# Kernel tuning notes

Measured on AMD Instinct MI355X. Metric: run time of the kernel, lower is better.

## Reference

```python
import jax, jax.numpy as jnp
import numpy as np

STATE_DIM, GOAL_DIM, OBST_DIM = 6, 3, 4
VEH_DIM = 2 * STATE_DIM + GOAL_DIM          # 15
IN_DIM = VEH_DIM + OBST_DIM                 # 19
HIDDEN = 256
ACT_DIM = 2
ACT_LIMIT = 1.0
LOG_STD_MIN, LOG_STD_MAX = -20.0, 2.0


def setup_inputs() -> dict:
    key = jax.random.key(0)
    ks = jax.random.split(key, 12)
    B, N = 512, 256
    sc = lambda fan_in: 1.0 / np.sqrt(fan_in)
    return {
        "obs": jax.random.normal(ks[0], (B, VEH_DIM), jnp.float32),
        "obstacles": jax.random.uniform(ks[1], (B, OBST_DIM + 1, N), jnp.float32),
        "eps": jax.random.normal(ks[2], (B, ACT_DIM), jnp.float32),
        "W1": jax.random.normal(ks[3], (IN_DIM, HIDDEN), jnp.float32) * sc(IN_DIM),
        "b1": jnp.zeros((HIDDEN,), jnp.float32),
        "W2": jax.random.normal(ks[4], (HIDDEN, HIDDEN), jnp.float32) * sc(HIDDEN),
        "b2": jnp.zeros((HIDDEN,), jnp.float32),
        "mu_W": jax.random.normal(ks[5], (HIDDEN, ACT_DIM), jnp.float32) * sc(HIDDEN),
        "mu_b": jnp.zeros((ACT_DIM,), jnp.float32),
        "ls_W": jax.random.normal(ks[6], (HIDDEN, ACT_DIM), jnp.float32) * sc(HIDDEN),
        "ls_b": jnp.zeros((ACT_DIM,), jnp.float32),
    }


def reference(obs, obstacles, eps, W1, b1, W2, b2, mu_W, mu_b, ls_W, ls_b):
    B, _, N = obstacles.shape
    # gather/expand/concat: [B, N, 19]
    veh = jnp.broadcast_to(obs[:, None, :], (B, N, VEH_DIM))
    obst_feats = jnp.swapaxes(obstacles[:, :OBST_DIM, :], 1, 2)  # [B, N, 4]
    x = jnp.concatenate([veh, obst_feats], axis=-1)
    # shared per-obstacle MLP (message function)
    h = jax.nn.relu(x @ W1 + b1)
    h = jax.nn.relu(h @ W2 + b2)                                 # [B, N, H]
    # masked sum pooling (aggregation)
    mask = obstacles[:, -1, :]                                   # [B, N]
    pooled = jnp.einsum('bnh,bn->bh', h, mask)                   # [B, H]
    # Gaussian tanh-squash head
    mu = pooled @ mu_W + mu_b
    log_std = jnp.clip(pooled @ ls_W + ls_b, LOG_STD_MIN, LOG_STD_MAX)
    std = jnp.exp(log_std)
    a = mu + std * eps  # rsample with externally supplied noise
    # Normal log_prob(a) with a = mu + std*eps  ->  -0.5*eps^2 - log_std - 0.5*log(2pi)
    logp = jnp.sum(-0.5 * eps * eps - log_std - 0.5 * jnp.log(2.0 * jnp.pi), axis=-1)
    # tanh correction
    logp = logp - jnp.sum(2.0 * (jnp.log(2.0) - a - jax.nn.softplus(-2.0 * a)), axis=-1)
    pi_action = ACT_LIMIT * jnp.tanh(a)
    return pi_action, logp
```

## Files before the change

### kernel.cpp

```cpp
#include <hip/hip_runtime.h>
#include <math.h>

typedef __attribute__((ext_vector_type(8))) short short8;
typedef __attribute__((ext_vector_type(4))) float f32x4;

__device__ __forceinline__ unsigned short f2bf(float x) {
    unsigned u = __float_as_uint(x);
    u += 0x7FFFu + ((u >> 16) & 1u);
    return (unsigned short)(u >> 16);
}

#define A1P_OFF 131072

__global__ __launch_bounds__(256) void prep_kernel(const float* __restrict__ W2,
                                                   const float* __restrict__ W1,
                                                   unsigned short* __restrict__ W2p,
                                                   unsigned short* __restrict__ A1p) {
    const int t = threadIdx.x;
    const int blk = blockIdx.x;
    if (blk < 32) {
        int f = blk * 256 + t;
        int l = f & 63, ct = (f >> 6) & 15, kt = f >> 10;
        int col = ct * 16 + (l & 15);
        int krow = kt * 32 + ((l >> 4) * 8);
        short8 v;
#pragma unroll
        for (int j = 0; j < 8; ++j) v[j] = (short)f2bf(W2[(krow + j) * 256 + col]);
        *reinterpret_cast<short8*>(W2p + (size_t)f * 8) = v;
    } else {
        int f = (blk - 32) * 256 + t;
        int l = f & 63, jt = f >> 6;
        int j = jt * 16 + (l & 15);
        short8 v;
#pragma unroll
        for (int jj = 0; jj < 8; ++jj) {
            int k = (l >> 4) * 8 + jj;
            v[jj] = (k < 4) ? (short)f2bf(W1[(15 + k) * 256 + j]) : (short)0;
        }
        *reinterpret_cast<short8*>(A1p + (size_t)f * 8) = v;
    }
}

__global__ __launch_bounds__(512, 2) void actor_kernel(
    const float* __restrict__ obs,  const float* __restrict__ obst,
    const float* __restrict__ W1,   const float* __restrict__ b1,
    const float* __restrict__ b2,   const unsigned short* __restrict__ W2p,
    const unsigned short* __restrict__ A1p,
    const float* __restrict__ muW,  const float* __restrict__ lsW,
    const float* __restrict__ mub,  const float* __restrict__ lsb,
    const float* __restrict__ eps,  float* __restrict__ out)
{
    __shared__ __align__(16) short sA[4 * 64 * 64];
    __shared__ float sVeh[256];
    __shared__ float sRed[8][4];

    const int b = blockIdx.x;
    const int t = threadIdx.x;
    const int l = t & 63;
    const int w = t >> 6;
    const int g = l >> 4;
    const int ln = l & 15;

    if (t < 256) {
        float a = b1[t];
#pragma unroll
        for (int i = 0; i < 15; ++i) a = fmaf(obs[b * 15 + i], W1[i * 256 + t], a);
        sVeh[t] = a;
    }

    short8 bfr[8][2];
#pragma unroll
    for (int kt = 0; kt < 8; ++kt)
#pragma unroll
        for (int c = 0; c < 2; ++c)
            bfr[kt][c] = *reinterpret_cast<const short8*>(
                W2p + (size_t)(((kt * 16 + (w * 2 + c)) * 64 + l) * 8));

    short8 a1[2];
#pragma unroll
    for (int ji = 0; ji < 2; ++ji)
        a1[ji] = *reinterpret_cast<const short8*>(
            A1p + (size_t)(((w * 2 + ji) * 64 + l) * 8));

    float bb[2]; float2 mwv[2], lwv[2];
#pragma unroll
    for (int c = 0; c < 2; ++c) {
        int col = w * 32 + c * 16 + ln;
        bb[c] = b2[col];
        mwv[c] = *reinterpret_cast<const float2*>(muW + col * 2);
        lwv[c] = *reinterpret_cast<const float2*>(lsW + col * 2);
    }

    const float* ob = obst + b * 1280;
    const float* maskbase = ob + 1024;

    short8 bf1[4];
    auto loadB1 = [&](int q) {
#pragma unroll
        for (int nt = 0; nt < 4; ++nt) {
            short8 v = {0, 0, 0, 0, 0, 0, 0, 0};
            if (l < 16) {
#pragma unroll
                for (int jj = 0; jj < 4; ++jj)
                    v[jj] = (short)f2bf(ob[jj * 256 + q * 64 + nt * 16 + l]);
            }
            bf1[nt] = v;
        }
    };
    loadB1(0);

    f32x4 acc[4][2];
#pragma unroll
    for (int m = 0; m < 4; ++m)
#pragma unroll
        for (int c = 0; c < 2; ++c) acc[m][c] = (f32x4){0.f, 0.f, 0.f, 0.f};
    float m0 = 0.f, m1 = 0.f, s0 = 0.f, s1 = 0.f;

    __syncthreads();

    for (int q = 0; q < 4; ++q) {
#pragma unroll
        for (int ji = 0; ji < 2; ++ji) {
            int jt = w * 2 + ji;
            int j0 = jt * 16 + g * 4;
            f32x4 bias = *reinterpret_cast<const f32x4*>(&sVeh[j0]);
            unsigned page = (unsigned)(j0 >> 6) * 8192;
            unsigned jbyte = (unsigned)((j0 & 63) * 2);
#pragma unroll
            for (int nt = 0; nt < 4; ++nt) {
                f32x4 d = (f32x4){0.f, 0.f, 0.f, 0.f};
                d = __builtin_amdgcn_mfma_f32_16x16x32_bf16(a1[ji], bf1[nt], d, 0, 0, 0);
                int n = nt * 16 + ln;
                unsigned p0 = (unsigned)f2bf(fmaxf(d[0] + bias[0], 0.f));
                unsigned p1 = (unsigned)f2bf(fmaxf(d[1] + bias[1], 0.f));
                unsigned p2 = (unsigned)f2bf(fmaxf(d[2] + bias[2], 0.f));
                unsigned p3 = (unsigned)f2bf(fmaxf(d[3] + bias[3], 0.f));
                uint2 u;
                u.x = p0 | (p1 << 16);
                u.y = p2 | (p3 << 16);
                unsigned off = page + (unsigned)(n * 128) + (jbyte ^ ((unsigned)((n & 7) << 4)));
                *reinterpret_cast<uint2*>((char*)sA + off) = u;
            }
        }
        if (q < 3) loadB1(q + 1);
        __syncthreads();

#pragma unroll
        for (int kt = 0; kt < 8; ++kt) {
            unsigned page = (unsigned)(kt >> 1) * 8192;
            unsigned kbyte = (unsigned)((kt & 1) * 64 + g * 16);
#pragma unroll
            for (int m = 0; m < 4; ++m) {
                int n = m * 16 + ln;
                unsigned off = page + (unsigned)(n * 128) + (kbyte ^ ((unsigned)((n & 7) << 4)));
                short8 afr = *reinterpret_cast<const short8*>((const char*)sA + off);
#pragma unroll
                for (int c = 0; c < 2; ++c)
                    acc[m][c] = __builtin_amdgcn_mfma_f32_16x16x32_bf16(afr, bfr[kt][c], acc[m][c], 0, 0, 0);
            }
        }

        const float* maskp = maskbase + q * 64;
#pragma unroll
        for (int c = 0; c < 2; ++c) {
            float p = 0.f;
#pragma unroll
            for (int m = 0; m < 4; ++m) {
                float4 M = *reinterpret_cast<const float4*>(maskp + m * 16 + g * 4);
                f32x4 v = acc[m][c];
                p = fmaf(M.x, fmaxf(v[0] + bb[c], 0.f), p);
                p = fmaf(M.y, fmaxf(v[1] + bb[c], 0.f), p);
                p = fmaf(M.z, fmaxf(v[2] + bb[c], 0.f), p);
                p = fmaf(M.w, fmaxf(v[3] + bb[c], 0.f), p);
                acc[m][c] = (f32x4){0.f, 0.f, 0.f, 0.f};
            }
            p += __shfl_xor(p, 16);
            p += __shfl_xor(p, 32);
            m0 = fmaf(p, mwv[c].x, m0);
            m1 = fmaf(p, mwv[c].y, m1);
            s0 = fmaf(p, lwv[c].x, s0);
            s1 = fmaf(p, lwv[c].y, s1);
        }
        if (q < 3) __syncthreads();
    }

#pragma unroll
    for (int off = 1; off < 16; off <<= 1) {
        m0 += __shfl_xor(m0, off);
        m1 += __shfl_xor(m1, off);
        s0 += __shfl_xor(s0, off);
        s1 += __shfl_xor(s1, off);
    }
    if (l == 0) { sRed[w][0] = m0; sRed[w][1] = m1; sRed[w][2] = s0; sRed[w][3] = s1; }
    __syncthreads();
    if (t == 0) {
        float M0 = 0.f, M1 = 0.f, S0 = 0.f, S1 = 0.f;
#pragma unroll
        for (int ww = 0; ww < 8; ++ww) {
            M0 += sRed[ww][0]; M1 += sRed[ww][1];
            S0 += sRed[ww][2]; S1 += sRed[ww][3];
        }
        float mu0 = M0 + mub[0], mu1 = M1 + mub[1];
        float ls0 = fminf(fmaxf(S0 + lsb[0], -20.f), 2.f);
        float ls1 = fminf(fmaxf(S1 + lsb[1], -20.f), 2.f);
        float e0 = eps[b * 2 + 0], e1 = eps[b * 2 + 1];
        float a0 = fmaf(expf(ls0), e0, mu0);
        float a1v = fmaf(expf(ls1), e1, mu1);
        float logp = -0.5f * (e0 * e0 + e1 * e1) - (ls0 + ls1) - 1.8378770664093453f;
        float x0 = -2.f * a0, x1 = -2.f * a1v;
        float sp0 = fmaxf(x0, 0.f) + log1pf(expf(-fabsf(x0)));
        float sp1 = fmaxf(x1, 0.f) + log1pf(expf(-fabsf(x1)));
        logp -= 2.f * (0.6931471805599453f - a0 - sp0);
        logp -= 2.f * (0.6931471805599453f - a1v - sp1);
        out[b * 2 + 0] = tanhf(a0);
        out[b * 2 + 1] = tanhf(a1v);
        out[1024 + b] = logp;
    }
}

extern "C" void kernel_launch(void* const* d_in, const int* in_sizes, int n_in,
                              void* d_out, int out_size, void* d_ws, size_t ws_size,
                              hipStream_t stream) {
    const float* obs  = (const float*)d_in[0];
    const float* obst = (const float*)d_in[1];
    const float* eps  = (const float*)d_in[2];
    const float* W1   = (const float*)d_in[3];
    const float* b1   = (const float*)d_in[4];
    const float* W2   = (const float*)d_in[5];
    const float* b2   = (const float*)d_in[6];
    const float* muW  = (const float*)d_in[7];
    const float* mub  = (const float*)d_in[8];
    const float* lsW  = (const float*)d_in[9];
    const float* lsb  = (const float*)d_in[10];
    float* out = (float*)d_out;

    char* ws = (char*)d_ws;
    unsigned short* W2p = (unsigned short*)ws;
    unsigned short* A1p = (unsigned short*)(ws + A1P_OFF);

    prep_kernel<<<36, 256, 0, stream>>>(W2, W1, W2p, A1p);
    actor_kernel<<<512, 512, 0, stream>>>(obs, obst, W1, b1, b2, W2p, A1p,
                                          muW, lsW, mub, lsb, eps, out);
}
```

Measured before the change: 37.00 us.

## Drop weight-prep kernel and convert fp32 weights to bf16 inside actor kernel

Removes the separate prep kernel that packed W2 and the obstacle part of W1 into bf16 MFMA-fragment layout. Each block now reads fp32 W2/W1 directly and converts with the packed hardware bf16 intrinsic, which also replaces the manual rounding in the hidden-layer store. Launch bounds change to ask for four blocks per CU. This saves a kernel launch and the dependency between the two kernels, but every one of 512 blocks now issues strided fp32 loads of the full W2 and converts it redundantly.

```diff
diff --git a/kernel.cpp b/kernel.cpp
--- a/kernel.cpp
+++ b/kernel.cpp
@@ -1,54 +1,24 @@
 #include <hip/hip_runtime.h>
+#include <hip/hip_bf16.h>
 #include <math.h>
 
 typedef __attribute__((ext_vector_type(8))) short short8;
 typedef __attribute__((ext_vector_type(4))) float f32x4;
 
-__device__ __forceinline__ unsigned short f2bf(float x) {
-    unsigned u = __float_as_uint(x);
-    u += 0x7FFFu + ((u >> 16) & 1u);
-    return (unsigned short)(u >> 16);
+__device__ __forceinline__ unsigned pkbf2(float lo, float hi) {
+    __hip_bfloat162 h = __float22bfloat162_rn(make_float2(lo, hi));
+    union { __hip_bfloat162 h; unsigned u; } c;
+    c.h = h;
+    return c.u;
 }
 
-#define A1P_OFF 131072
-
-__global__ __launch_bounds__(256) void prep_kernel(const float* __restrict__ W2,
-                                                   const float* __restrict__ W1,
-                                                   unsigned short* __restrict__ W2p,
-                                                   unsigned short* __restrict__ A1p) {
-    const int t = threadIdx.x;
-    const int blk = blockIdx.x;
-    if (blk < 32) {
-        int f = blk * 256 + t;
-        int l = f & 63, ct = (f >> 6) & 15, kt = f >> 10;
-        int col = ct * 16 + (l & 15);
-        int krow = kt * 32 + ((l >> 4) * 8);
-        short8 v;
-#pragma unroll
-        for (int j = 0; j < 8; ++j) v[j] = (short)f2bf(W2[(krow + j) * 256 + col]);
-        *reinterpret_cast<short8*>(W2p + (size_t)f * 8) = v;
-    } else {
-        int f = (blk - 32) * 256 + t;
-        int l = f & 63, jt = f >> 6;
-        int j = jt * 16 + (l & 15);
-        short8 v;
-#pragma unroll
-        for (int jj = 0; jj < 8; ++jj) {
-            int k = (l >> 4) * 8 + jj;
-            v[jj] = (k < 4) ? (short)f2bf(W1[(15 + k) * 256 + j]) : (short)0;
-        }
-        *reinterpret_cast<short8*>(A1p + (size_t)f * 8) = v;
-    }
-}
-
-__global__ __launch_bounds__(512, 2) void actor_kernel(
+__global__ __launch_bounds__(512, 4) void actor_kernel(
     const float* __restrict__ obs,  const float* __restrict__ obst,
-    const float* __restrict__ W1,   const float* __restrict__ b1,
-    const float* __restrict__ b2,   const unsigned short* __restrict__ W2p,
-    const unsigned short* __restrict__ A1p,
-    const float* __restrict__ muW,  const float* __restrict__ lsW,
-    const float* __restrict__ mub,  const float* __restrict__ lsb,
-    const float* __restrict__ eps,  float* __restrict__ out)
+    const float* __restrict__ eps,  const float* __restrict__ W1,
+    const float* __restrict__ b1,   const float* __restrict__ W2,
+    const float* __restrict__ b2,   const float* __restrict__ muW,
+    const float* __restrict__ mub,  const float* __restrict__ lsW,
+    const float* __restrict__ lsb,  float* __restrict__ out)
 {
     __shared__ __align__(16) short sA[4 * 64 * 64];
     __shared__ float sVeh[256];
@@ -70,17 +40,33 @@
 
     short8 bfr[8][2];
 #pragma unroll
-    for (int kt = 0; kt < 8; ++kt)
-#pragma unroll
-        for (int c = 0; c < 2; ++c)
-            bfr[kt][c] = *reinterpret_cast<const short8*>(
-                W2p + (size_t)(((kt * 16 + (w * 2 + c)) * 64 + l) * 8));
+    for (int kt = 0; kt < 8; ++kt) {
+#pragma unroll
+        for (int c = 0; c < 2; ++c) {
+            const float* p = W2 + (size_t)(kt * 32 + g * 8) * 256 + (w * 2 + c) * 16 + ln;
+            float f0 = p[0 * 256], f1 = p[1 * 256], f2 = p[2 * 256], f3 = p[3 * 256];
+            float f4 = p[4 * 256], f5 = p[5 * 256], f6 = p[6 * 256], f7 = p[7 * 256];
+            union { short8 s; unsigned u[4]; } tv;
+            tv.u[0] = pkbf2(f0, f1);
+            tv.u[1] = pkbf2(f2, f3);
+            tv.u[2] = pkbf2(f4, f5);
+            tv.u[3] = pkbf2(f6, f7);
+            bfr[kt][c] = tv.s;
+        }
+    }
 
     short8 a1[2];
 #pragma unroll
-    for (int ji = 0; ji < 2; ++ji)
-        a1[ji] = *reinterpret_cast<const short8*>(
-            A1p + (size_t)(((w * 2 + ji) * 64 + l) * 8));
+    for (int ji = 0; ji < 2; ++ji) {
+        union { short8 s; unsigned u[4]; } tv;
+        tv.u[0] = 0u; tv.u[1] = 0u; tv.u[2] = 0u; tv.u[3] = 0u;
+        if (g == 0) {
+            int j = (w * 2 + ji) * 16 + ln;
+            tv.u[0] = pkbf2(W1[15 * 256 + j], W1[16 * 256 + j]);
+            tv.u[1] = pkbf2(W1[17 * 256 + j], W1[18 * 256 + j]);
+        }
+        a1[ji] = tv.s;
+    }
 
     float bb[2]; float2 mwv[2], lwv[2];
 #pragma unroll
@@ -98,13 +84,14 @@
     auto loadB1 = [&](int q) {
 #pragma unroll
         for (int nt = 0; nt < 4; ++nt) {
-            short8 v = {0, 0, 0, 0, 0, 0, 0, 0};
+            union { short8 s; unsigned u[4]; } tv;
+            tv.u[0] = 0u; tv.u[1] = 0u; tv.u[2] = 0u; tv.u[3] = 0u;
             if (l < 16) {
-#pragma unroll
-                for (int jj = 0; jj < 4; ++jj)
-                    v[jj] = (short)f2bf(ob[jj * 256 + q * 64 + nt * 16 + l]);
-            }
-            bf1[nt] = v;
+                const float* pp = ob + q * 64 + nt * 16 + l;
+                tv.u[0] = pkbf2(pp[0], pp[256]);
+                tv.u[1] = pkbf2(pp[512], pp[768]);
+            }
+            bf1[nt] = tv.s;
         }
     };
     loadB1(0);
@@ -131,13 +118,9 @@
                 f32x4 d = (f32x4){0.f, 0.f, 0.f, 0.f};
                 d = __builtin_amdgcn_mfma_f32_16x16x32_bf16(a1[ji], bf1[nt], d, 0, 0, 0);
                 int n = nt * 16 + ln;
-                unsigned p0 = (unsigned)f2bf(fmaxf(d[0] + bias[0], 0.f));
-                unsigned p1 = (unsigned)f2bf(fmaxf(d[1] + bias[1], 0.f));
-                unsigned p2 = (unsigned)f2bf(fmaxf(d[2] + bias[2], 0.f));
-                unsigned p3 = (unsigned)f2bf(fmaxf(d[3] + bias[3], 0.f));
                 uint2 u;
-                u.x = p0 | (p1 << 16);
-                u.y = p2 | (p3 << 16);
+                u.x = pkbf2(fmaxf(d[0] + bias[0], 0.f), fmaxf(d[1] + bias[1], 0.f));
+                u.y = pkbf2(fmaxf(d[2] + bias[2], 0.f), fmaxf(d[3] + bias[3], 0.f));
                 unsigned off = page + (unsigned)(n * 128) + (jbyte ^ ((unsigned)((n & 7) << 4)));
                 *reinterpret_cast<uint2*>((char*)sA + off) = u;
             }
@@ -234,11 +217,6 @@
     const float* lsb  = (const float*)d_in[10];
     float* out = (float*)d_out;
 
-    char* ws = (char*)d_ws;
-    unsigned short* W2p = (unsigned short*)ws;
-    unsigned short* A1p = (unsigned short*)(ws + A1P_OFF);
-
-    prep_kernel<<<36, 256, 0, stream>>>(W2, W1, W2p, A1p);
-    actor_kernel<<<512, 512, 0, stream>>>(obs, obst, W1, b1, b2, W2p, A1p,
-                                          muW, lsW, mub, lsb, eps, out);
+    actor_kernel<<<512, 512, 0, stream>>>(obs, obst, eps, W1, b1, W2, b2,
+                                          muW, mub, lsW, lsb, out);
 }
```

Result: slower. 60.47 us (+63.4%).
